# Optimization experiments

Hardware: AMD Instinct MI355X
Metric: run time of the kernel (lower is better)

## Reference

```python
import jax, jax.numpy as jnp
import numpy as np

N = 50000      # num nodes
E = 600000     # num edges (avg degree 12)
IN = 256       # in_feats
H = 128        # h_feats
P = 2          # prop_step
LN_EPS = 1e-5


def setup_inputs() -> dict:
    key = jax.random.key(0)
    ks = jax.random.split(key, 8)
    return {
        "in_feat": jax.random.normal(ks[0], (N, IN), jnp.float32),
        "row": jax.random.randint(ks[1], (E,), 0, N),  # target node of each edge
        "col": jax.random.randint(ks[2], (E,), 0, N),  # source node of each edge
        "lin_w": jax.random.normal(ks[3], (H, IN), jnp.float32) / np.sqrt(IN).astype(np.float32),
        "lin_b": jnp.zeros((H,), jnp.float32),
        "conv_w": jax.random.normal(ks[4], (H, H), jnp.float32) / np.sqrt(H).astype(np.float32),
        "conv_b": jnp.zeros((H,), jnp.float32),
        "root_emb": jax.random.normal(ks[5], (1, H), jnp.float32) * 0.02,
        "ln_gamma": jnp.ones((P, H), jnp.float32),
        "ln_beta": jnp.zeros((P, H), jnp.float32),
    }


def _layernorm(x, g, b):
    mu = jnp.mean(x, axis=-1, keepdims=True)
    var = jnp.mean(jnp.square(x - mu), axis=-1, keepdims=True)
    return (x - mu) * jax.lax.rsqrt(var + LN_EPS) * g + b


def reference(in_feat, row, col, lin_w, lin_b, conv_w, conv_b, root_emb, ln_gamma, ln_beta):
    n = in_feat.shape[0]
    h = in_feat @ lin_w.T + lin_b                      # [N, H]

    # OGB-style degree norm with +1 trick (original edges, row = target)
    deg = jax.ops.segment_sum(jnp.ones_like(row, dtype=h.dtype), row, num_segments=n) + 1.0
    deg_inv = 1.0 / deg                                # deg >= 1, never inf

    # GCNConv symmetric norm with self loops: D^-1/2 (A+I) D^-1/2
    loop = jnp.arange(n)
    r2 = jnp.concatenate([row, loop])                  # [E+N] targets
    c2 = jnp.concatenate([col, loop])                  # [E+N] sources
    d2 = jax.ops.segment_sum(jnp.ones_like(r2, dtype=h.dtype), r2, num_segments=n)
    dis = jnp.where(d2 > 0, jax.lax.rsqrt(jnp.maximum(d2, 1.0)), 0.0)
    ew = dis[r2] * dis[c2]                             # [E+N] edge weights

    root = root_emb[0]                                 # [H]
    ori = h
    for i in range(P):
        if i != 0:
            h = h + ori                                # residual
            h = _layernorm(h, ln_gamma[i], ln_beta[i])
            h = jax.nn.relu(h)
            # dropout=0.0 -> identity
        xw = h @ conv_w.T                              # [N, H]
        h_msg = jax.ops.segment_sum(ew[:, None] * xw[c2], r2, num_segments=n) + conv_b
        root_contrib = jax.nn.relu(h + root) * deg_inv[:, None]
        h = h_msg + root_contrib
    return h
```

## Files before the change

kernel.cpp:

```cpp
#include <hip/hip_runtime.h>

#define NN 50000
#define EE 600000
#define INF 256
#define HF 128
#define CEB ((EE + 255) / 256)

typedef __attribute__((ext_vector_type(8))) short short8;
typedef __attribute__((ext_vector_type(4))) float floatx4;

__device__ __forceinline__ unsigned short f32_to_bf16_rne(float x) {
    unsigned int u = __float_as_uint(x);
    unsigned int r = (u + 0x7FFFu + ((u >> 16) & 1u)) >> 16;
    return (unsigned short)r;
}
__device__ __forceinline__ float bf16_to_f32(unsigned short h) {
    return __uint_as_float(((unsigned int)h) << 16);
}
__device__ __forceinline__ float bf16lo_u32(unsigned int u) {
    return __uint_as_float(u << 16);
}
__device__ __forceinline__ float bf16hi_u32(unsigned int u) {
    return __uint_as_float(u & 0xFFFF0000u);
}
__device__ __forceinline__ void cvt_hilo8(float4 v0, float4 v1, short8& hs, short8& ls) {
    float x[8] = {v0.x, v0.y, v0.z, v0.w, v1.x, v1.y, v1.z, v1.w};
    union { short8 s; unsigned short u[8]; } H, L;
#pragma unroll
    for (int k = 0; k < 8; ++k) {
        unsigned short hi = f32_to_bf16_rne(x[k]);
        H.u[k] = hi;
        L.u[k] = f32_to_bf16_rne(x[k] - bf16_to_f32(hi));
    }
    hs = H.s;
    ls = L.s;
}

__global__ void count_and_prepack(const int* __restrict__ row, int* __restrict__ cnt,
                                  int* __restrict__ pos, int E,
                                  const float* __restrict__ lw, const float* __restrict__ cw,
                                  unsigned short* __restrict__ fl, unsigned short* __restrict__ fc) {
    int b = blockIdx.x;
    if (b < CEB) {
        int e = b * 256 + threadIdx.x;
        if (e < E) pos[e] = atomicAdd(&cnt[row[e]], 1);
        return;
    }
    int idx = (b - CEB) * 256 + threadIdx.x;
    const float* src;
    unsigned short* dst;
    int K, c;
    if (idx < 8192) {
        src = lw; dst = fl; K = INF; c = idx;
    } else if (idx < 12288) {
        src = cw; dst = fc; K = HF; c = idx - 8192;
    } else return;
    int lane = c & 63;
    int nt = (c >> 6) & 7;
    int hl = (c >> 9) & 1;
    int kc = c >> 10;
    int rw = nt * 16 + (lane & 15);
    int koff = kc * 32 + (lane >> 4) * 8;
    const float* p = &src[(size_t)rw * K + koff];
    float4 v0 = *reinterpret_cast<const float4*>(p);
    float4 v1 = *reinterpret_cast<const float4*>(p + 4);
    short8 hs, ls;
    cvt_hilo8(v0, v1, hs, ls);
    *reinterpret_cast<short8*>(&dst[(size_t)c * 8]) = hl ? ls : hs;
}

__global__ void scan_phase1(const int* __restrict__ cnt, int* __restrict__ bsum, int n) {
    __shared__ int sdata[256];
    int t = threadIdx.x;
    int i = blockIdx.x * 256 + t;
    sdata[t] = (i < n) ? cnt[i] : 0;
    __syncthreads();
    for (int s = 128; s > 0; s >>= 1) {
        if (t < s) sdata[t] += sdata[t + s];
        __syncthreads();
    }
    if (t == 0) bsum[blockIdx.x] = sdata[0];
}

__global__ void scan_phase3(const int* __restrict__ cnt, const int* __restrict__ bsum,
                            int* __restrict__ row_start,
                            float* __restrict__ deg_inv, float* __restrict__ dis,
                            int n, int nb, int E) {
    __shared__ int sb[256];
    __shared__ int sdata[256];
    int t = threadIdx.x;
    sb[t] = (t < nb) ? bsum[t] : 0;
    __syncthreads();
    for (int s = 1; s < 256; s <<= 1) {
        int add = (t >= s) ? sb[t - s] : 0;
        __syncthreads();
        sb[t] += add;
        __syncthreads();
    }
    int base = sb[blockIdx.x] - bsum[blockIdx.x];
    int i = blockIdx.x * 256 + t;
    int v = (i < n) ? cnt[i] : 0;
    sdata[t] = v;
    __syncthreads();
    for (int s = 1; s < 256; s <<= 1) {
        int add = (t >= s) ? sdata[t - s] : 0;
        __syncthreads();
        sdata[t] += add;
        __syncthreads();
    }
    if (i < n) {
        int ex = base + sdata[t] - v;
        row_start[i] = ex;
        float d = (float)(v + 1);
        deg_inv[i] = 1.0f / d;
        dis[i] = rsqrtf(d);
    }
    if (blockIdx.x == 0 && t == 0) row_start[n] = E;
}

__global__ void fill_csr(const int* __restrict__ row, const int* __restrict__ col,
                         const int* __restrict__ row_start, const int* __restrict__ pos,
                         int* __restrict__ csr_col, int E) {
    int e = blockIdx.x * blockDim.x + threadIdx.x;
    if (e < E) {
        int p = row_start[row[e]] + pos[e];
        __builtin_nontemporal_store(col[e], &csr_col[p]);
    }
}

template <int K, int MODE>
__global__ __launch_bounds__(256) void gemm_ldsw(
    const float* __restrict__ Af,
    const unsigned short* __restrict__ Ahg, const unsigned short* __restrict__ Alg,
    const unsigned short* __restrict__ Wf,
    const float* __restrict__ bias,
    float* __restrict__ C, unsigned short* __restrict__ Cbf,
    const float* __restrict__ h, const float* __restrict__ deg_inv,
    const float* __restrict__ dis, const float* __restrict__ root,
    const float* __restrict__ gamma, const float* __restrict__ beta,
    int M) {
    constexpr int NKC = K / 32;
    __shared__ unsigned short WS[2 * 8192];

    const int t = threadIdx.x;
    const int wave = t >> 6;
    const int lane = t & 63;
    const int lrow = lane & 15;
    const int quad = lane >> 4;
    const int bm = blockIdx.x * 64;
    int arow = bm + wave * 16 + lrow;
    if (arow >= M) arow = M - 1;

    floatx4 acc[8];
#pragma unroll
    for (int nt = 0; nt < 8; ++nt) acc[nt] = (floatx4){0.f, 0.f, 0.f, 0.f};

#pragma unroll
    for (int p = 0; p < NKC / 2; ++p) {
        if (p) __syncthreads();
        {
            const uint4* src = reinterpret_cast<const uint4*>(Wf + (size_t)p * 16384);
            uint4* dstl = reinterpret_cast<uint4*>(WS);
#pragma unroll
            for (int i = 0; i < 8; ++i) dstl[t + 256 * i] = src[t + 256 * i];
        }
        __syncthreads();
#pragma unroll
        for (int k2 = 0; k2 < 2; ++k2) {
            int kc = p * 2 + k2;
            short8 afh, afl;
            if (MODE == 0) {
                const float* ap = &Af[(size_t)arow * K + kc * 32 + quad * 8];
                float4 a0 = *reinterpret_cast<const float4*>(ap);
                float4 a1 = *reinterpret_cast<const float4*>(ap + 4);
                cvt_hilo8(a0, a1, afh, afl);
            } else {
                size_t ao = (size_t)arow * K + kc * 32 + quad * 8;
                afh = *reinterpret_cast<const short8*>(&Ahg[ao]);
                afl = *reinterpret_cast<const short8*>(&Alg[ao]);
            }
            const unsigned short* wb = &WS[k2 * 8192 + lane * 8];
#pragma unroll
            for (int nt = 0; nt < 8; ++nt) {
                short8 bfh = *reinterpret_cast<const short8*>(wb + nt * 512);
                short8 bfl = *reinterpret_cast<const short8*>(wb + 4096 + nt * 512);
                acc[nt] = __builtin_amdgcn_mfma_f32_16x16x32_bf16(afh, bfh, acc[nt], 0, 0, 0);
                acc[nt] = __builtin_amdgcn_mfma_f32_16x16x32_bf16(afl, bfh, acc[nt], 0, 0, 0);
                acc[nt] = __builtin_amdgcn_mfma_f32_16x16x32_bf16(afh, bfl, acc[nt], 0, 0, 0);
            }
        }
    }

    float cb[8], rt[8], gm[8], bt[8];
#pragma unroll
    for (int nt = 0; nt < 8; ++nt) {
        int colh = nt * 16 + lrow;
        cb[nt] = bias[colh];
        if (MODE >= 1) rt[nt] = root[colh];
        if (MODE == 1) { gm[nt] = gamma[colh]; bt[nt] = beta[colh]; }
    }

#pragma unroll
    for (int r = 0; r < 4; ++r) {
        int grow = bm + wave * 16 + quad * 4 + r;
        bool ok = (grow < M);
        int gr = ok ? grow : M - 1;
        float x[8];
        if (MODE == 0) {
#pragma unroll
            for (int nt = 0; nt < 8; ++nt) x[nt] = acc[nt][r] + cb[nt];
        } else {
            float di = deg_inv[gr];
            float hv[8];
#pragma unroll
            for (int nt = 0; nt < 8; ++nt) hv[nt] = h[(size_t)gr * HF + nt * 16 + lrow];
#pragma unroll
            for (int nt = 0; nt < 8; ++nt) {
                float v = acc[nt][r] + cb[nt] + fmaxf(hv[nt] + rt[nt], 0.f) * di;
                x[nt] = (MODE == 1) ? v + hv[nt] : v;
            }
        }
        if (MODE == 1) {
            float s = 0.f;
#pragma unroll
            for (int nt = 0; nt < 8; ++nt) s += x[nt];
#pragma unroll
            for (int m = 1; m < 16; m <<= 1) s += __shfl_xor(s, m, 64);
            float mu = s * (1.0f / HF);
            float var = 0.f;
#pragma unroll
            for (int nt = 0; nt < 8; ++nt) { float d = x[nt] - mu; var += d * d; }
#pragma unroll
            for (int m = 1; m < 16; m <<= 1) var += __shfl_xor(var, m, 64);
            float rs = rsqrtf(var * (1.0f / HF) + 1e-5f);
            float ds = dis[gr];
            if (ok) {
#pragma unroll
                for (int nt = 0; nt < 8; ++nt) {
                    int colh = nt * 16 + lrow;
                    float y = fmaxf((x[nt] - mu) * rs * gm[nt] + bt[nt], 0.f);
                    C[(size_t)grow * HF + colh] = y;
                    Cbf[(size_t)grow * HF + colh] = f32_to_bf16_rne(ds * y);
                }
            }
        } else if (MODE == 0) {
            if (ok) {
                float ds = dis[grow];
#pragma unroll
                for (int nt = 0; nt < 8; ++nt) {
                    int colh = nt * 16 + lrow;
                    C[(size_t)grow * HF + colh] = x[nt];
                    Cbf[(size_t)grow * HF + colh] = f32_to_bf16_rne(ds * x[nt]);
                }
            }
        } else {
            if (ok) {
#pragma unroll
                for (int nt = 0; nt < 8; ++nt)
                    C[(size_t)grow * HF + nt * 16 + lrow] = x[nt];
            }
        }
    }
}

__global__ void aggregate(const int* __restrict__ row_start, const int* __restrict__ csr_col,
                          const float* __restrict__ dis, const float* __restrict__ deg_inv,
                          const float* __restrict__ h, const unsigned short* __restrict__ hbf,
                          unsigned short* __restrict__ agg_hi, unsigned short* __restrict__ agg_lo,
                          int n) {
    int wid = (blockIdx.x * blockDim.x + threadIdx.x) >> 6;
    int lane = threadIdx.x & 63;
    if (wid >= n) return;
    int q = lane >> 4;
    int l16 = lane & 15;
    int s = row_start[wid];
    int e = row_start[wid + 1];
    float a0 = 0.f, a1 = 0.f, a2 = 0.f, a3 = 0.f, a4 = 0.f, a5 = 0.f, a6 = 0.f, a7 = 0.f;
    if (e - s <= 16) {
        int j0 = s + q;
        bool p0 = j0 < e, p1 = j0 + 4 < e, p2 = j0 + 8 < e, p3 = j0 + 12 < e;
        int c0 = p0 ? csr_col[j0] : 0;
        int c1 = p1 ? csr_col[j0 + 4] : 0;
        int c2 = p2 ? csr_col[j0 + 8] : 0;
        int c3 = p3 ? csr_col[j0 + 12] : 0;
        uint4 z = make_uint4(0, 0, 0, 0);
        uint4 g0 = z, g1 = z, g2 = z, g3 = z;
        if (p0) g0 = *reinterpret_cast<const uint4*>(&hbf[(size_t)c0 * HF + l16 * 8]);
        if (p1) g1 = *reinterpret_cast<const uint4*>(&hbf[(size_t)c1 * HF + l16 * 8]);
        if (p2) g2 = *reinterpret_cast<const uint4*>(&hbf[(size_t)c2 * HF + l16 * 8]);
        if (p3) g3 = *reinterpret_cast<const uint4*>(&hbf[(size_t)c3 * HF + l16 * 8]);
        a0 = bf16lo_u32(g0.x) + bf16lo_u32(g1.x) + bf16lo_u32(g2.x) + bf16lo_u32(g3.x);
        a1 = bf16hi_u32(g0.x) + bf16hi_u32(g1.x) + bf16hi_u32(g2.x) + bf16hi_u32(g3.x);
        a2 = bf16lo_u32(g0.y) + bf16lo_u32(g1.y) + bf16lo_u32(g2.y) + bf16lo_u32(g3.y);
        a3 = bf16hi_u32(g0.y) + bf16hi_u32(g1.y) + bf16hi_u32(g2.y) + bf16hi_u32(g3.y);
        a4 = bf16lo_u32(g0.z) + bf16lo_u32(g1.z) + bf16lo_u32(g2.z) + bf16lo_u32(g3.z);
        a5 = bf16hi_u32(g0.z) + bf16hi_u32(g1.z) + bf16hi_u32(g2.z) + bf16hi_u32(g3.z);
        a6 = bf16lo_u32(g0.w) + bf16lo_u32(g1.w) + bf16lo_u32(g2.w) + bf16lo_u32(g3.w);
        a7 = bf16hi_u32(g0.w) + bf16hi_u32(g1.w) + bf16hi_u32(g2.w) + bf16hi_u32(g3.w);
    } else {
        float b0 = 0.f, b1 = 0.f, b2 = 0.f, b3 = 0.f, b4 = 0.f, b5 = 0.f, b6 = 0.f, b7 = 0.f;
        int j = s + q;
        for (; j + 4 < e; j += 8) {
            int c0 = csr_col[j];
            int c1 = csr_col[j + 4];
            uint4 h0 = *reinterpret_cast<const uint4*>(&hbf[(size_t)c0 * HF + l16 * 8]);
            uint4 h1 = *reinterpret_cast<const uint4*>(&hbf[(size_t)c1 * HF + l16 * 8]);
            a0 += bf16lo_u32(h0.x); a1 += bf16hi_u32(h0.x);
            a2 += bf16lo_u32(h0.y); a3 += bf16hi_u32(h0.y);
            a4 += bf16lo_u32(h0.z); a5 += bf16hi_u32(h0.z);
            a6 += bf16lo_u32(h0.w); a7 += bf16hi_u32(h0.w);
            b0 += bf16lo_u32(h1.x); b1 += bf16hi_u32(h1.x);
            b2 += bf16lo_u32(h1.y); b3 += bf16hi_u32(h1.y);
            b4 += bf16lo_u32(h1.z); b5 += bf16hi_u32(h1.z);
            b6 += bf16lo_u32(h1.w); b7 += bf16hi_u32(h1.w);
        }
        if (j < e) {
            int c0 = csr_col[j];
            uint4 h0 = *reinterpret_cast<const uint4*>(&hbf[(size_t)c0 * HF + l16 * 8]);
            a0 += bf16lo_u32(h0.x); a1 += bf16hi_u32(h0.x);
            a2 += bf16lo_u32(h0.y); a3 += bf16hi_u32(h0.y);
            a4 += bf16lo_u32(h0.z); a5 += bf16hi_u32(h0.z);
            a6 += bf16lo_u32(h0.w); a7 += bf16hi_u32(h0.w);
        }
        a0 += b0; a1 += b1; a2 += b2; a3 += b3;
        a4 += b4; a5 += b5; a6 += b6; a7 += b7;
    }
#pragma unroll
    for (int m = 16; m < 64; m <<= 1) {
        a0 += __shfl_xor(a0, m, 64);
        a1 += __shfl_xor(a1, m, 64);
        a2 += __shfl_xor(a2, m, 64);
        a3 += __shfl_xor(a3, m, 64);
        a4 += __shfl_xor(a4, m, 64);
        a5 += __shfl_xor(a5, m, 64);
        a6 += __shfl_xor(a6, m, 64);
        a7 += __shfl_xor(a7, m, 64);
    }
    if (q == 0) {
        float dn = dis[wid];
        float di = deg_inv[wid];
        float4 hA = *reinterpret_cast<const float4*>(&h[(size_t)wid * HF + l16 * 8]);
        float4 hB = *reinterpret_cast<const float4*>(&h[(size_t)wid * HF + l16 * 8 + 4]);
        float o[8];
        o[0] = fmaf(dn, a0, di * hA.x);
        o[1] = fmaf(dn, a1, di * hA.y);
        o[2] = fmaf(dn, a2, di * hA.z);
        o[3] = fmaf(dn, a3, di * hA.w);
        o[4] = fmaf(dn, a4, di * hB.x);
        o[5] = fmaf(dn, a5, di * hB.y);
        o[6] = fmaf(dn, a6, di * hB.z);
        o[7] = fmaf(dn, a7, di * hB.w);
        unsigned short hi[8], lo[8];
#pragma unroll
        for (int k = 0; k < 8; ++k) {
            hi[k] = f32_to_bf16_rne(o[k]);
            lo[k] = f32_to_bf16_rne(o[k] - bf16_to_f32(hi[k]));
        }
        uint4 hp, lp;
        hp.x = (unsigned)hi[0] | ((unsigned)hi[1] << 16);
        hp.y = (unsigned)hi[2] | ((unsigned)hi[3] << 16);
        hp.z = (unsigned)hi[4] | ((unsigned)hi[5] << 16);
        hp.w = (unsigned)hi[6] | ((unsigned)hi[7] << 16);
        lp.x = (unsigned)lo[0] | ((unsigned)lo[1] << 16);
        lp.y = (unsigned)lo[2] | ((unsigned)lo[3] << 16);
        lp.z = (unsigned)lo[4] | ((unsigned)lo[5] << 16);
        lp.w = (unsigned)lo[6] | ((unsigned)lo[7] << 16);
        *reinterpret_cast<uint4*>(&agg_hi[(size_t)wid * HF + l16 * 8]) = hp;
        *reinterpret_cast<uint4*>(&agg_lo[(size_t)wid * HF + l16 * 8]) = lp;
    }
}

extern "C" void kernel_launch(void* const* d_in, const int* in_sizes, int n_in,
                              void* d_out, int out_size, void* d_ws, size_t ws_size,
                              hipStream_t stream) {
    const int N = NN, E = EE;
    const float* in_feat = (const float*)d_in[0];
    const int* row = (const int*)d_in[1];
    const int* col = (const int*)d_in[2];
    const float* lin_w = (const float*)d_in[3];
    const float* lin_b = (const float*)d_in[4];
    const float* conv_w = (const float*)d_in[5];
    const float* conv_b = (const float*)d_in[6];
    const float* root_emb = (const float*)d_in[7];
    const float* ln_gamma = (const float*)d_in[8];
    const float* ln_beta = (const float*)d_in[9];
    float* out = (float*)d_out;

    float* ws = (float*)d_ws;
    size_t o = 0;
    float* deg_inv = ws + o; o += N;
    float* dis = ws + o; o += N;
    int* cnt = (int*)(ws + o); o += N;
    int* row_start = (int*)(ws + o); o += N + 4;
    int* pos = (int*)(ws + o); o += E;
    int* bsum = (int*)(ws + o); o += 256;
    int* csr_col = (int*)(ws + o); o += E;
    o = (o + 3) & ~(size_t)3;
    unsigned short* fl = (unsigned short*)(ws + o); o += 32768;
    unsigned short* fc = (unsigned short*)(ws + o); o += 16384;
    float* h0 = ws + o; o += (size_t)N * HF;
    unsigned short* hbf = (unsigned short*)(ws + o); o += (size_t)N * HF / 2;
    unsigned short* agg_hi = (unsigned short*)(ws + o); o += (size_t)N * HF / 2;
    unsigned short* agg_lo = (unsigned short*)(ws + o); o += (size_t)N * HF / 2;

    const int NB = (N + 255) / 256;

    hipMemsetAsync(cnt, 0, N * sizeof(int), stream);
    count_and_prepack<<<CEB + 48, 256, 0, stream>>>(row, cnt, pos, E, lin_w, conv_w, fl, fc);
    scan_phase1<<<NB, 256, 0, stream>>>(cnt, bsum, N);
    scan_phase3<<<NB, 256, 0, stream>>>(cnt, bsum, row_start, deg_inv, dis, N, NB, E);
    fill_csr<<<CEB, 256, 0, stream>>>(row, col, row_start, pos, csr_col, E);

    const int GB = (N + 63) / 64;
    const int WB = (N + 3) / 4;

    gemm_ldsw<INF, 0><<<GB, 256, 0, stream>>>(in_feat, nullptr, nullptr, fl, lin_b,
                                              h0, hbf, nullptr, nullptr, dis, nullptr,
                                              nullptr, nullptr, N);

    aggregate<<<WB, 256, 0, stream>>>(row_start, csr_col, dis, deg_inv, h0, hbf,
                                      agg_hi, agg_lo, N);
    gemm_ldsw<HF, 1><<<GB, 256, 0, stream>>>(nullptr, agg_hi, agg_lo, fc, conv_b,
                                             h0, hbf, h0, deg_inv, dis, root_emb,
                                             ln_gamma + HF, ln_beta + HF, N);

    aggregate<<<WB, 256, 0, stream>>>(row_start, csr_col, dis, deg_inv, h0, hbf,
                                      agg_hi, agg_lo, N);
    gemm_ldsw<HF, 2><<<GB, 256, 0, stream>>>(nullptr, agg_hi, agg_lo, fc, conv_b,
                                             out, nullptr, h0, deg_inv, dis, root_emb,
                                             nullptr, nullptr, N);
}
```

Measured before the change: 290.3 us.

## Fuse first GEMM with degree counting and convert weights inside GEMM

The input linear GEMM is merged into one launch with the edge-counting atomics. It no longer depends on the degree scan, so source-side dis scaling moves from the GEMM epilogue into the aggregation loop as a per-edge multiply. The separate weight prepack kernel is removed, and each GEMM block now converts fp32 weights to hi/lo bf16 in LDS itself. This cuts launches and serialization but adds redundant weight conversion per block and an extra dis gather per edge.

```diff
diff --git a/kernel.cpp b/kernel.cpp
--- a/kernel.cpp
+++ b/kernel.cpp
@@ -5,6 +5,8 @@
 #define INF 256
 #define HF 128
 #define CEB ((EE + 255) / 256)
+#define GB ((NN + 63) / 64)
+#define NBCH ((NN + 255) / 256)
 
 typedef __attribute__((ext_vector_type(8))) short short8;
 typedef __attribute__((ext_vector_type(4))) float floatx4;
@@ -34,39 +36,6 @@
     }
     hs = H.s;
     ls = L.s;
-}
-
-__global__ void count_and_prepack(const int* __restrict__ row, int* __restrict__ cnt,
-                                  int* __restrict__ pos, int E,
-                                  const float* __restrict__ lw, const float* __restrict__ cw,
-                                  unsigned short* __restrict__ fl, unsigned short* __restrict__ fc) {
-    int b = blockIdx.x;
-    if (b < CEB) {
-        int e = b * 256 + threadIdx.x;
-        if (e < E) pos[e] = atomicAdd(&cnt[row[e]], 1);
-        return;
-    }
-    int idx = (b - CEB) * 256 + threadIdx.x;
-    const float* src;
-    unsigned short* dst;
-    int K, c;
-    if (idx < 8192) {
-        src = lw; dst = fl; K = INF; c = idx;
-    } else if (idx < 12288) {
-        src = cw; dst = fc; K = HF; c = idx - 8192;
-    } else return;
-    int lane = c & 63;
-    int nt = (c >> 6) & 7;
-    int hl = (c >> 9) & 1;
-    int kc = c >> 10;
-    int rw = nt * 16 + (lane & 15);
-    int koff = kc * 32 + (lane >> 4) * 8;
-    const float* p = &src[(size_t)rw * K + koff];
-    float4 v0 = *reinterpret_cast<const float4*>(p);
-    float4 v1 = *reinterpret_cast<const float4*>(p + 4);
-    short8 hs, ls;
-    cvt_hilo8(v0, v1, hs, ls);
-    *reinterpret_cast<short8*>(&dst[(size_t)c * 8]) = hl ? ls : hs;
 }
 
 __global__ void scan_phase1(const int* __restrict__ cnt, int* __restrict__ bsum, int n) {
@@ -109,8 +78,7 @@
         __syncthreads();
     }
     if (i < n) {
-        int ex = base + sdata[t] - v;
-        row_start[i] = ex;
+        row_start[i] = base + sdata[t] - v;
         float d = (float)(v + 1);
         deg_inv[i] = 1.0f / d;
         dis[i] = rsqrtf(d);
@@ -129,25 +97,24 @@
 }
 
 template <int K, int MODE>
-__global__ __launch_bounds__(256) void gemm_ldsw(
+__device__ __forceinline__ void gemm_tile(
+    int bidx,
     const float* __restrict__ Af,
     const unsigned short* __restrict__ Ahg, const unsigned short* __restrict__ Alg,
-    const unsigned short* __restrict__ Wf,
+    const float* __restrict__ Wsrc,
     const float* __restrict__ bias,
     float* __restrict__ C, unsigned short* __restrict__ Cbf,
     const float* __restrict__ h, const float* __restrict__ deg_inv,
-    const float* __restrict__ dis, const float* __restrict__ root,
+    const float* __restrict__ root,
     const float* __restrict__ gamma, const float* __restrict__ beta,
-    int M) {
+    unsigned short* WS, int M) {
     constexpr int NKC = K / 32;
-    __shared__ unsigned short WS[2 * 8192];
-
     const int t = threadIdx.x;
     const int wave = t >> 6;
     const int lane = t & 63;
     const int lrow = lane & 15;
     const int quad = lane >> 4;
-    const int bm = blockIdx.x * 64;
+    const int bm = bidx * 64;
     int arow = bm + wave * 16 + lrow;
     if (arow >= M) arow = M - 1;
 
@@ -156,18 +123,28 @@
     for (int nt = 0; nt < 8; ++nt) acc[nt] = (floatx4){0.f, 0.f, 0.f, 0.f};
 
 #pragma unroll
-    for (int p = 0; p < NKC / 2; ++p) {
-        if (p) __syncthreads();
-        {
-            const uint4* src = reinterpret_cast<const uint4*>(Wf + (size_t)p * 16384);
-            uint4* dstl = reinterpret_cast<uint4*>(WS);
-#pragma unroll
-            for (int i = 0; i < 8; ++i) dstl[t + 256 * i] = src[t + 256 * i];
+    for (int pp = 0; pp < NKC / 2; ++pp) {
+        if (pp) __syncthreads();
+#pragma unroll
+        for (int u0 = 0; u0 < 4; ++u0) {
+            int u = t + u0 * 256;
+            int kc2 = u >> 9;
+            int nt = (u >> 6) & 7;
+            int ln = u & 63;
+            int rw = nt * 16 + (ln & 15);
+            int koff = (pp * 2 + kc2) * 32 + (ln >> 4) * 8;
+            const float* p = &Wsrc[(size_t)rw * K + koff];
+            float4 v0 = *reinterpret_cast<const float4*>(p);
+            float4 v1 = *reinterpret_cast<const float4*>(p + 4);
+            short8 hs, ls;
+            cvt_hilo8(v0, v1, hs, ls);
+            *reinterpret_cast<short8*>(&WS[kc2 * 8192 + nt * 512 + ln * 8]) = hs;
+            *reinterpret_cast<short8*>(&WS[kc2 * 8192 + 4096 + nt * 512 + ln * 8]) = ls;
         }
         __syncthreads();
 #pragma unroll
         for (int k2 = 0; k2 < 2; ++k2) {
-            int kc = p * 2 + k2;
+            int kc = pp * 2 + k2;
             short8 afh, afl;
             if (MODE == 0) {
                 const float* ap = &Af[(size_t)arow * K + kc * 32 + quad * 8];
@@ -233,24 +210,22 @@
 #pragma unroll
             for (int m = 1; m < 16; m <<= 1) var += __shfl_xor(var, m, 64);
             float rs = rsqrtf(var * (1.0f / HF) + 1e-5f);
-            float ds = dis[gr];
             if (ok) {
 #pragma unroll
                 for (int nt = 0; nt < 8; ++nt) {
                     int colh = nt * 16 + lrow;
                     float y = fmaxf((x[nt] - mu) * rs * gm[nt] + bt[nt], 0.f);
                     C[(size_t)grow * HF + colh] = y;
-                    Cbf[(size_t)grow * HF + colh] = f32_to_bf16_rne(ds * y);
+                    Cbf[(size_t)grow * HF + colh] = f32_to_bf16_rne(y);
                 }
             }
         } else if (MODE == 0) {
             if (ok) {
-                float ds = dis[grow];
 #pragma unroll
                 for (int nt = 0; nt < 8; ++nt) {
                     int colh = nt * 16 + lrow;
                     C[(size_t)grow * HF + colh] = x[nt];
-                    Cbf[(size_t)grow * HF + colh] = f32_to_bf16_rne(ds * x[nt]);
+                    Cbf[(size_t)grow * HF + colh] = f32_to_bf16_rne(x[nt]);
                 }
             }
         } else {
@@ -261,6 +236,36 @@
             }
         }
     }
+}
+
+__global__ __launch_bounds__(256) void gemm0_count(
+    const float* __restrict__ in_feat, const float* __restrict__ lin_w,
+    const float* __restrict__ lin_b,
+    float* __restrict__ h0, unsigned short* __restrict__ hbf,
+    const int* __restrict__ row, int* __restrict__ cnt, int* __restrict__ pos) {
+    __shared__ unsigned short WS[2 * 8192];
+    int b = blockIdx.x;
+    if (b < GB) {
+        gemm_tile<INF, 0>(b, in_feat, nullptr, nullptr, lin_w, lin_b,
+                          h0, hbf, nullptr, nullptr, nullptr,
+                          nullptr, nullptr, WS, NN);
+        return;
+    }
+    int e = (b - GB) * 256 + threadIdx.x;
+    if (e < EE) pos[e] = atomicAdd(&cnt[row[e]], 1);
+}
+
+template <int MODE>
+__global__ __launch_bounds__(256) void gemm_conv(
+    const unsigned short* __restrict__ agg_hi, const unsigned short* __restrict__ agg_lo,
+    const float* __restrict__ conv_w, const float* __restrict__ conv_b,
+    float* __restrict__ C, unsigned short* __restrict__ Cbf,
+    const float* __restrict__ h, const float* __restrict__ deg_inv,
+    const float* __restrict__ root,
+    const float* __restrict__ gamma, const float* __restrict__ beta) {
+    __shared__ unsigned short WS[2 * 8192];
+    gemm_tile<HF, MODE>(blockIdx.x, nullptr, agg_hi, agg_lo, conv_w, conv_b,
+                        C, Cbf, h, deg_inv, root, gamma, beta, WS, NN);
 }
 
 __global__ void aggregate(const int* __restrict__ row_start, const int* __restrict__ csr_col,
@@ -283,44 +288,48 @@
         int c1 = p1 ? csr_col[j0 + 4] : 0;
         int c2 = p2 ? csr_col[j0 + 8] : 0;
         int c3 = p3 ? csr_col[j0 + 12] : 0;
+        float d0 = dis[c0], d1 = dis[c1], d2 = dis[c2], d3 = dis[c3];
         uint4 z = make_uint4(0, 0, 0, 0);
         uint4 g0 = z, g1 = z, g2 = z, g3 = z;
         if (p0) g0 = *reinterpret_cast<const uint4*>(&hbf[(size_t)c0 * HF + l16 * 8]);
         if (p1) g1 = *reinterpret_cast<const uint4*>(&hbf[(size_t)c1 * HF + l16 * 8]);
         if (p2) g2 = *reinterpret_cast<const uint4*>(&hbf[(size_t)c2 * HF + l16 * 8]);
         if (p3) g3 = *reinterpret_cast<const uint4*>(&hbf[(size_t)c3 * HF + l16 * 8]);
-        a0 = bf16lo_u32(g0.x) + bf16lo_u32(g1.x) + bf16lo_u32(g2.x) + bf16lo_u32(g3.x);
-        a1 = bf16hi_u32(g0.x) + bf16hi_u32(g1.x) + bf16hi_u32(g2.x) + bf16hi_u32(g3.x);
-        a2 = bf16lo_u32(g0.y) + bf16lo_u32(g1.y) + bf16lo_u32(g2.y) + bf16lo_u32(g3.y);
-        a3 = bf16hi_u32(g0.y) + bf16hi_u32(g1.y) + bf16hi_u32(g2.y) + bf16hi_u32(g3.y);
-        a4 = bf16lo_u32(g0.z) + bf16lo_u32(g1.z) + bf16lo_u32(g2.z) + bf16lo_u32(g3.z);
-        a5 = bf16hi_u32(g0.z) + bf16hi_u32(g1.z) + bf16hi_u32(g2.z) + bf16hi_u32(g3.z);
-        a6 = bf16lo_u32(g0.w) + bf16lo_u32(g1.w) + bf16lo_u32(g2.w) + bf16lo_u32(g3.w);
-        a7 = bf16hi_u32(g0.w) + bf16hi_u32(g1.w) + bf16hi_u32(g2.w) + bf16hi_u32(g3.w);
+        a0 = d0 * bf16lo_u32(g0.x) + d1 * bf16lo_u32(g1.x) + d2 * bf16lo_u32(g2.x) + d3 * bf16lo_u32(g3.x);
+        a1 = d0 * bf16hi_u32(g0.x) + d1 * bf16hi_u32(g1.x) + d2 * bf16hi_u32(g2.x) + d3 * bf16hi_u32(g3.x);
+        a2 = d0 * bf16lo_u32(g0.y) + d1 * bf16lo_u32(g1.y) + d2 * bf16lo_u32(g2.y) + d3 * bf16lo_u32(g3.y);
+        a3 = d0 * bf16hi_u32(g0.y) + d1 * bf16hi_u32(g1.y) + d2 * bf16hi_u32(g2.y) + d3 * bf16hi_u32(g3.y);
+        a4 = d0 * bf16lo_u32(g0.z) + d1 * bf16lo_u32(g1.z) + d2 * bf16lo_u32(g2.z) + d3 * bf16lo_u32(g3.z);
+        a5 = d0 * bf16hi_u32(g0.z) + d1 * bf16hi_u32(g1.z) + d2 * bf16hi_u32(g2.z) + d3 * bf16hi_u32(g3.z);
+        a6 = d0 * bf16lo_u32(g0.w) + d1 * bf16lo_u32(g1.w) + d2 * bf16lo_u32(g2.w) + d3 * bf16lo_u32(g3.w);
+        a7 = d0 * bf16hi_u32(g0.w) + d1 * bf16hi_u32(g1.w) + d2 * bf16hi_u32(g2.w) + d3 * bf16hi_u32(g3.w);
     } else {
         float b0 = 0.f, b1 = 0.f, b2 = 0.f, b3 = 0.f, b4 = 0.f, b5 = 0.f, b6 = 0.f, b7 = 0.f;
         int j = s + q;
         for (; j + 4 < e; j += 8) {
             int c0 = csr_col[j];
             int c1 = csr_col[j + 4];
+            float d0 = dis[c0];
+            float d1 = dis[c1];
             uint4 h0 = *reinterpret_cast<const uint4*>(&hbf[(size_t)c0 * HF + l16 * 8]);
             uint4 h1 = *reinterpret_cast<const uint4*>(&hbf[(size_t)c1 * HF + l16 * 8]);
-            a0 += bf16lo_u32(h0.x); a1 += bf16hi_u32(h0.x);
-            a2 += bf16lo_u32(h0.y); a3 += bf16hi_u32(h0.y);
-            a4 += bf16lo_u32(h0.z); a5 += bf16hi_u32(h0.z);
-            a6 += bf16lo_u32(h0.w); a7 += bf16hi_u32(h0.w);
-            b0 += bf16lo_u32(h1.x); b1 += bf16hi_u32(h1.x);
-            b2 += bf16lo_u32(h1.y); b3 += bf16hi_u32(h1.y);
-            b4 += bf16lo_u32(h1.z); b5 += bf16hi_u32(h1.z);
-            b6 += bf16lo_u32(h1.w); b7 += bf16hi_u32(h1.w);
+            a0 = fmaf(d0, bf16lo_u32(h0.x), a0); a1 = fmaf(d0, bf16hi_u32(h0.x), a1);
+            a2 = fmaf(d0, bf16lo_u32(h0.y), a2); a3 = fmaf(d0, bf16hi_u32(h0.y), a3);
+            a4 = fmaf(d0, bf16lo_u32(h0.z), a4); a5 = fmaf(d0, bf16hi_u32(h0.z), a5);
+            a6 = fmaf(d0, bf16lo_u32(h0.w), a6); a7 = fmaf(d0, bf16hi_u32(h0.w), a7);
+            b0 = fmaf(d1, bf16lo_u32(h1.x), b0); b1 = fmaf(d1, bf16hi_u32(h1.x), b1);
+            b2 = fmaf(d1, bf16lo_u32(h1.y), b2); b3 = fmaf(d1, bf16hi_u32(h1.y), b3);
+            b4 = fmaf(d1, bf16lo_u32(h1.z), b4); b5 = fmaf(d1, bf16hi_u32(h1.z), b5);
+            b6 = fmaf(d1, bf16lo_u32(h1.w), b6); b7 = fmaf(d1, bf16hi_u32(h1.w), b7);
         }
         if (j < e) {
             int c0 = csr_col[j];
+            float d0 = dis[c0];
             uint4 h0 = *reinterpret_cast<const uint4*>(&hbf[(size_t)c0 * HF + l16 * 8]);
-            a0 += bf16lo_u32(h0.x); a1 += bf16hi_u32(h0.x);
-            a2 += bf16lo_u32(h0.y); a3 += bf16hi_u32(h0.y);
-            a4 += bf16lo_u32(h0.z); a5 += bf16hi_u32(h0.z);
-            a6 += bf16lo_u32(h0.w); a7 += bf16hi_u32(h0.w);
+            a0 = fmaf(d0, bf16lo_u32(h0.x), a0); a1 = fmaf(d0, bf16hi_u32(h0.x), a1);
+            a2 = fmaf(d0, bf16lo_u32(h0.y), a2); a3 = fmaf(d0, bf16hi_u32(h0.y), a3);
+            a4 = fmaf(d0, bf16lo_u32(h0.z), a4); a5 = fmaf(d0, bf16hi_u32(h0.z), a5);
+            a6 = fmaf(d0, bf16lo_u32(h0.w), a6); a7 = fmaf(d0, bf16hi_u32(h0.w), a7);
         }
         a0 += b0; a1 += b1; a2 += b2; a3 += b3;
         a4 += b4; a5 += b5; a6 += b6; a7 += b7;
@@ -395,38 +404,29 @@
     int* pos = (int*)(ws + o); o += E;
     int* bsum = (int*)(ws + o); o += 256;
     int* csr_col = (int*)(ws + o); o += E;
-    o = (o + 3) & ~(size_t)3;
-    unsigned short* fl = (unsigned short*)(ws + o); o += 32768;
-    unsigned short* fc = (unsigned short*)(ws + o); o += 16384;
     float* h0 = ws + o; o += (size_t)N * HF;
     unsigned short* hbf = (unsigned short*)(ws + o); o += (size_t)N * HF / 2;
     unsigned short* agg_hi = (unsigned short*)(ws + o); o += (size_t)N * HF / 2;
     unsigned short* agg_lo = (unsigned short*)(ws + o); o += (size_t)N * HF / 2;
 
-    const int NB = (N + 255) / 256;
+    const int WB = (N + 3) / 4;
 
     hipMemsetAsync(cnt, 0, N * sizeof(int), stream);
-    count_and_prepack<<<CEB + 48, 256, 0, stream>>>(row, cnt, pos, E, lin_w, conv_w, fl, fc);
-    scan_phase1<<<NB, 256, 0, stream>>>(cnt, bsum, N);
-    scan_phase3<<<NB, 256, 0, stream>>>(cnt, bsum, row_start, deg_inv, dis, N, NB, E);
+
+    gemm0_count<<<GB + CEB, 256, 0, stream>>>(in_feat, lin_w, lin_b, h0, hbf,
+                                              row, cnt, pos);
+    scan_phase1<<<NBCH, 256, 0, stream>>>(cnt, bsum, N);
+    scan_phase3<<<NBCH, 256, 0, stream>>>(cnt, bsum, row_start, deg_inv, dis, N, NBCH, E);
     fill_csr<<<CEB, 256, 0, stream>>>(row, col, row_start, pos, csr_col, E);
-
-    const int GB = (N + 63) / 64;
-    const int WB = (N + 3) / 4;
-
-    gemm_ldsw<INF, 0><<<GB, 256, 0, stream>>>(in_feat, nullptr, nullptr, fl, lin_b,
-                                              h0, hbf, nullptr, nullptr, dis, nullptr,
-                                              nullptr, nullptr, N);
 
     aggregate<<<WB, 256, 0, stream>>>(row_start, csr_col, dis, deg_inv, h0, hbf,
                                       agg_hi, agg_lo, N);
-    gemm_ldsw<HF, 1><<<GB, 256, 0, stream>>>(nullptr, agg_hi, agg_lo, fc, conv_b,
-                                             h0, hbf, h0, deg_inv, dis, root_emb,
-                                             ln_gamma + HF, ln_beta + HF, N);
+    gemm_conv<1><<<GB, 256, 0, stream>>>(agg_hi, agg_lo, conv_w, conv_b, h0, hbf,
+                                         h0, deg_inv, root_emb,
+                                         ln_gamma + HF, ln_beta + HF);
 
     aggregate<<<WB, 256, 0, stream>>>(row_start, csr_col, dis, deg_inv, h0, hbf,
                                       agg_hi, agg_lo, N);
-    gemm_ldsw<HF, 2><<<GB, 256, 0, stream>>>(nullptr, agg_hi, agg_lo, fc, conv_b,
-                                             out, nullptr, h0, deg_inv, dis, root_emb,
-                                             nullptr, nullptr, N);
-}
+    gemm_conv<2><<<GB, 256, 0, stream>>>(agg_hi, agg_lo, conv_w, conv_b, out, nullptr,
+                                         h0, deg_inv, root_emb, nullptr, nullptr);
+}
```

Result: no change. 285.5 us (-1.7%).
